# Kernel tuning notes

Hardware: AMD Instinct MI355X
Metric: run time of the kernel (lower is better)

Reference implementation:

```python
import jax, jax.numpy as jnp
import numpy as np
import math

DIM = 4096
N_HEADS = 32
N_KV_HEADS = 8
HEAD_DIM = DIM // N_HEADS  # 128
N_REP = N_HEADS // N_KV_HEADS  # 4
BATCH = 1
SEQ = 2048
ROPE_THETA = 10000.0


def setup_inputs() -> dict:
    key = jax.random.key(0)
    ks = jax.random.split(key, 6)
    x = jax.random.normal(ks[0], (BATCH, SEQ, DIM), dtype=jnp.float32)
    # torch nn.Linear weights are [out_features, in_features]
    s = 1.0 / math.sqrt(DIM)
    wq = jax.random.normal(ks[1], (N_HEADS * HEAD_DIM, DIM), dtype=jnp.float32) * s
    wk = jax.random.normal(ks[2], (N_KV_HEADS * HEAD_DIM, DIM), dtype=jnp.float32) * s
    wv = jax.random.normal(ks[3], (N_KV_HEADS * HEAD_DIM, DIM), dtype=jnp.float32) * s
    wo = jax.random.normal(ks[4], (DIM, N_HEADS * HEAD_DIM), dtype=jnp.float32) * s
    # precomputed rotary frequencies (real/imag parts of freqs_cis)
    inv_freq = 1.0 / (ROPE_THETA ** (jnp.arange(0, HEAD_DIM, 2, dtype=jnp.float32) / HEAD_DIM))
    t = jnp.arange(SEQ, dtype=jnp.float32)
    freqs = jnp.outer(t, inv_freq)  # [S, HEAD_DIM//2]
    return {"x": x, "wq": wq, "wk": wk, "wv": wv, "wo": wo,
            "freqs_cos": jnp.cos(freqs), "freqs_sin": jnp.sin(freqs)}


def _apply_rotary(t, cos, sin):
    # t: [B, S, H, HD]; cos/sin: [S, HD//2]
    B, S, H, HD = t.shape
    tr = t.reshape(B, S, H, HD // 2, 2)
    re, im = tr[..., 0], tr[..., 1]
    c = cos[None, :, None, :]
    s = sin[None, :, None, :]
    out_re = re * c - im * s
    out_im = re * s + im * c
    return jnp.stack([out_re, out_im], axis=-1).reshape(B, S, H, HD)


def reference(x, wq, wk, wv, wo, freqs_cos, freqs_sin):
    B, S, _ = x.shape
    q = jnp.einsum('bsd,od->bso', x, wq).reshape(B, S, N_HEADS, HEAD_DIM)
    k = jnp.einsum('bsd,od->bso', x, wk).reshape(B, S, N_KV_HEADS, HEAD_DIM)
    v = jnp.einsum('bsd,od->bso', x, wv).reshape(B, S, N_KV_HEADS, HEAD_DIM)
    q = _apply_rotary(q, freqs_cos, freqs_sin)
    k = _apply_rotary(k, freqs_cos, freqs_sin)
    # repeat kv heads (GQA): [B,S,Hkv,HD] -> [B,S,H,HD]
    k = jnp.repeat(k, N_REP, axis=2)
    v = jnp.repeat(v, N_REP, axis=2)
    # SDPA with causal mask
    scale = 1.0 / math.sqrt(HEAD_DIM)
    scores = jnp.einsum('bqhd,bkhd->bhqk', q, k) * scale
    causal = jnp.tril(jnp.ones((S, S), dtype=bool))
    scores = jnp.where(causal[None, None], scores, jnp.finfo(scores.dtype).min)
    attn = jax.nn.softmax(scores, axis=-1)
    y = jnp.einsum('bhqk,bkhd->bqhd', attn, v).reshape(B, S, N_HEADS * HEAD_DIM)
    return jnp.einsum('bso,do->bsd', y, wo)
```

## Files before the change

kernel.cpp:

```cpp
#include <hip/hip_runtime.h>
#include <hip/hip_bf16.h>
#include <stdint.h>

typedef unsigned short u16;
typedef __bf16 bf16_8 __attribute__((ext_vector_type(8)));
typedef float f32x4 __attribute__((ext_vector_type(4)));

#define SEQ 2048
#define DIM 4096
#define NH 32
#define NKV 8
#define HD 128
#define QSCALE_LOG2E 0.12753785222167917f

__device__ inline u16 f2bf(float f) {
    unsigned int u = __float_as_uint(f);
    unsigned int r = (u + 0x7fffu + ((u >> 16) & 1u)) >> 16;
    return (u16)r;
}

__device__ inline void async16(const void* g, void* l) {
    __builtin_amdgcn_global_load_lds(
        (const __attribute__((address_space(1))) void*)g,
        (__attribute__((address_space(3))) void*)l, 16, 0, 0);
}

__global__ __launch_bounds__(256) void cast_all(const float* __restrict__ x,
                                                const float* __restrict__ wq,
                                                const float* __restrict__ wk,
                                                const float* __restrict__ wv,
                                                const float* __restrict__ wo,
                                                u16* __restrict__ dst) {
    size_t i4 = (size_t)blockIdx.x * 256 + threadIdx.x;
    size_t e = i4 * 4;
    const float* src;
    size_t off;
    if (e < 8388608ull)       { src = x;  off = 0; }
    else if (e < 25165824ull) { src = wq; off = 8388608ull; }
    else if (e < 29360128ull) { src = wk; off = 25165824ull; }
    else if (e < 33554432ull) { src = wv; off = 29360128ull; }
    else                      { src = wo; off = 33554432ull; }
    float4 v = ((const float4*)src)[i4 - off / 4];
    ushort4 o;
    o.x = f2bf(v.x); o.y = f2bf(v.y); o.z = f2bf(v.z); o.w = f2bf(v.w);
    ((ushort4*)dst)[i4] = o;
}

template <int MODE>
__global__ __launch_bounds__(512, 2) void gemm8p(const u16* __restrict__ A,
                                                 const u16* __restrict__ B,
                                                 void* __restrict__ C0,
                                                 void* __restrict__ C1,
                                                 void* __restrict__ C2,
                                                 const float* __restrict__ fc,
                                                 const float* __restrict__ fs,
                                                 int M, int N, int K) {
    extern __shared__ u16 sm[];
    u16* As = sm;
    u16* Bs = sm + 3 * 128 * 64;

    const int tid = threadIdx.x;
    const int lane = tid & 63;
    const int wid = tid >> 6;
    const int wr = wid >> 2;
    const int wc = wid & 3;
    const int quad = lane >> 4;
    const int l16 = lane & 15;

    const int nwg = gridDim.x * gridDim.y;
    int id = blockIdx.y * gridDim.x + blockIdx.x;
    int swz = (id & 7) * (nwg >> 3) + (id >> 3);
    const int bm = (swz / gridDim.x) * 128;
    const int bn = (swz % gridDim.x) * 256;

    f32x4 acc[4][4] = {};

    auto stage = [&](int sb, int t) {
        const int k0 = t << 6;
        {
            int s0 = wc * 64 + lane;
#pragma unroll
            for (int r = 0; r < 2; ++r) {
                int S = r * 256 + s0;
                int row = S >> 3, sl = S & 7;
                int ch = sl ^ (row & 7);
                const u16* g = &A[(size_t)(bm + wr * 64 + row) * K + k0 + ch * 8];
                async16(g, (void*)&As[sb * (128 * 64) + wr * (64 * 64) + S * 8]);
            }
        }
        {
            int s0 = wr * 64 + lane;
#pragma unroll
            for (int r = 0; r < 4; ++r) {
                int S = r * 128 + s0;
                int row = S >> 3, sl = S & 7;
                int ch = sl ^ (row & 7);
                const u16* g = &B[(size_t)(bn + wc * 64 + row) * K + k0 + ch * 8];
                async16(g, (void*)&Bs[sb * (256 * 64) + wc * (64 * 64) + S * 8]);
            }
        }
    };

    const int chsw = l16 & 7;
    auto compute = [&](int p) {
        const u16* as = As + p * (128 * 64) + wr * (64 * 64);
        const u16* bs = Bs + p * (256 * 64) + wc * (64 * 64);
#pragma unroll
        for (int ks = 0; ks < 2; ++ks) {
            const int slot = ((ks * 4 + quad) ^ chsw) * 8;
            bf16_8 a[4], b[4];
#pragma unroll
            for (int i = 0; i < 4; ++i)
                a[i] = *(const bf16_8*)&as[(i * 16 + l16) * 64 + slot];
#pragma unroll
            for (int j = 0; j < 4; ++j)
                b[j] = *(const bf16_8*)&bs[(j * 16 + l16) * 64 + slot];
            __builtin_amdgcn_s_setprio(1);
#pragma unroll
            for (int i = 0; i < 4; ++i)
#pragma unroll
                for (int j = 0; j < 4; ++j)
                    acc[i][j] = __builtin_amdgcn_mfma_f32_16x16x32_bf16(a[i], b[j], acc[i][j], 0, 0, 0);
            __builtin_amdgcn_s_setprio(0);
        }
    };

    const int NT = K >> 6;
    stage(0, 0);
    stage(1, 1);

    int p = 0;
    for (int t = 0; t < NT - 2; ++t) {
        int sb = p + 2; if (sb >= 3) sb -= 3;
        stage(sb, t + 2);
        asm volatile("s_waitcnt vmcnt(12)" ::: "memory");
        __builtin_amdgcn_s_barrier();
        compute(p);
        __builtin_amdgcn_s_barrier();
        p = (p == 2) ? 0 : p + 1;
    }
    asm volatile("s_waitcnt vmcnt(6)" ::: "memory");
    __builtin_amdgcn_s_barrier();
    compute(p);
    __builtin_amdgcn_s_barrier();
    p = (p == 2) ? 0 : p + 1;
    asm volatile("s_waitcnt vmcnt(0)" ::: "memory");
    __builtin_amdgcn_s_barrier();
    compute(p);

    const int wm = wr * 64;
    const int wn = wc * 64;

    if (MODE == 0) {
        float* Cf = (float*)C0;
#pragma unroll
        for (int i = 0; i < 4; ++i)
#pragma unroll
            for (int j = 0; j < 4; ++j)
#pragma unroll
                for (int r = 0; r < 4; ++r)
                    Cf[(size_t)(bm + wm + i * 16 + quad * 4 + r) * N + (bn + wn + j * 16 + l16)] =
                        acc[i][j][r];
    } else {
        u16* Qb = (u16*)C0;
        u16* Kb = (u16*)C1;
        u16* Vt = (u16*)C2;
        if (bn < 5120) {
            const bool isQ = bn < 4096;
            const float osc = isQ ? QSCALE_LOG2E : 1.0f;
#pragma unroll
            for (int i = 0; i < 4; ++i)
#pragma unroll
                for (int j = 0; j < 4; ++j) {
                    int n = bn + wn + j * 16 + l16;
                    int pp = (n & 127) >> 1;
                    bool odd = (l16 & 1);
#pragma unroll
                    for (int r = 0; r < 4; ++r) {
                        int m = bm + wm + i * 16 + quad * 4 + r;
                        float v = acc[i][j][r];
                        float u = __shfl_xor(v, 1);
                        float c = fc[m * 64 + pp];
                        float s = fs[m * 64 + pp];
                        float o = (odd ? (u * s + v * c) : (v * c - u * s)) * osc;
                        if (isQ)
                            Qb[(size_t)m * 4096 + n] = f2bf(o);
                        else
                            Kb[(size_t)m * 1024 + (n - 4096)] = f2bf(o);
                    }
                }
        } else {
#pragma unroll
            for (int i = 0; i < 4; ++i)
#pragma unroll
                for (int j = 0; j < 4; ++j) {
                    int n = bn + wn + j * 16 + l16;
                    ushort4 o;
                    o.x = f2bf(acc[i][j][0]);
                    o.y = f2bf(acc[i][j][1]);
                    o.z = f2bf(acc[i][j][2]);
                    o.w = f2bf(acc[i][j][3]);
                    *(ushort4*)&Vt[(size_t)(n - 5120) * SEQ + (bm + wm + i * 16 + quad * 4)] = o;
                }
        }
    }
}

__global__ __launch_bounds__(256, 4) void attn_k(const u16* __restrict__ Q,
                                                 const u16* __restrict__ Kb,
                                                 const u16* __restrict__ Vt,
                                                 u16* __restrict__ Y) {
    __shared__ u16 Ks[64 * 128];
    __shared__ u16 Vs[128 * 64];
    __shared__ u16 Ps[4 * 16 * 64];
    const int tid = threadIdx.x;
    const int lane = tid & 63;
    const int w = tid >> 6;
    const int quad = lane >> 4;
    const int l16 = lane & 15;
    const int id = blockIdx.x;
    const int qt = 31 - (id >> 5);
    const int h = id & 31;
    const int kvh = h >> 2;
    const size_t qrow0 = (size_t)qt * 64;

    bf16_8 qf[4];
#pragma unroll
    for (int ks = 0; ks < 4; ++ks)
        qf[ks] = *(const bf16_8*)&Q[(qrow0 + w * 16 + l16) * DIM + h * HD + ks * 32 + quad * 8];

    f32x4 po[8] = {};
    float lsum = 0.f;

    char* psbase = (char*)Ps + w * 2048 + l16 * 128;
    const int sw = (l16 & 7) << 1;

    for (int kt = 0; kt <= qt; ++kt) {
#pragma unroll
        for (int r = 0; r < 4; ++r) {
            int S = r * 256 + tid;
            {
                int row = S >> 4, slot = S & 15;
                int chunk = slot ^ (row & 15);
                const char* g = (const char*)Kb +
                    (((size_t)kt * 64 + row) * 1024 + kvh * HD + chunk * 8) * 2;
                async16(g, (char*)Ks + S * 16);
            }
            {
                int row = S >> 3, slot = S & 7;
                int chunk = slot ^ (row & 7);
                const char* g = (const char*)Vt +
                    (((size_t)(kvh * HD + row)) * SEQ + kt * 64 + chunk * 8) * 2;
                async16(g, (char*)Vs + S * 16);
            }
        }
        __syncthreads();

        f32x4 sc[4] = {};
#pragma unroll
        for (int ks = 0; ks < 4; ++ks)
#pragma unroll
            for (int jb = 0; jb < 4; ++jb) {
                bf16_8 kb = *(const bf16_8*)&Ks[(jb * 16 + l16) * 128 + ((ks * 4 + quad) ^ l16) * 8];
                sc[jb] = __builtin_amdgcn_mfma_f32_16x16x32_bf16(kb, qf[ks], sc[jb], 0, 0, 0);
            }

        float pv[4][4];
#pragma unroll
        for (int jb = 0; jb < 4; ++jb)
#pragma unroll
            for (int r = 0; r < 4; ++r)
                pv[jb][r] = exp2f(sc[jb][r]);

        if (kt == qt) {
            int qloc = w * 16 + l16;
#pragma unroll
            for (int jb = 0; jb < 4; ++jb)
#pragma unroll
                for (int r = 0; r < 4; ++r)
                    if (jb * 16 + quad * 4 + r > qloc) pv[jb][r] = 0.f;
        }

#pragma unroll
        for (int jb = 0; jb < 4; ++jb) {
            lsum += (pv[jb][0] + pv[jb][1]) + (pv[jb][2] + pv[jb][3]);
            ushort4 pk;
            pk.x = f2bf(pv[jb][0]);
            pk.y = f2bf(pv[jb][1]);
            pk.z = f2bf(pv[jb][2]);
            pk.w = f2bf(pv[jb][3]);
            int c = jb * 4 + quad;
            *(ushort4*)(psbase + ((c ^ sw) << 3)) = pk;
        }

#pragma unroll
        for (int ks = 0; ks < 2; ++ks) {
            int c = ks * 8 + quad * 2;
            bf16_8 pf = *(const bf16_8*)(psbase + ((c ^ sw) << 3));
#pragma unroll
            for (int n = 0; n < 8; ++n) {
                bf16_8 vf = *(const bf16_8*)&Vs[(n * 16 + l16) * 64 + (((ks * 4 + quad) ^ (l16 & 7))) * 8];
                po[n] = __builtin_amdgcn_mfma_f32_16x16x32_bf16(pf, vf, po[n], 0, 0, 0);
            }
        }
        __syncthreads();
    }

    lsum += __shfl_xor(lsum, 16);
    lsum += __shfl_xor(lsum, 32);
    float inv = 1.f / lsum;
#pragma unroll
    for (int r = 0; r < 4; ++r) {
        float invr = __shfl(inv, quad * 4 + r);
        size_t row = qrow0 + w * 16 + quad * 4 + r;
#pragma unroll
        for (int n = 0; n < 8; ++n)
            Y[row * DIM + h * HD + n * 16 + l16] = f2bf(po[n][r] * invr);
    }
}

extern "C" void kernel_launch(void* const* d_in, const int* in_sizes, int n_in,
                              void* d_out, int out_size, void* d_ws, size_t ws_size,
                              hipStream_t stream) {
    const float* x  = (const float*)d_in[0];
    const float* wq = (const float*)d_in[1];
    const float* wk = (const float*)d_in[2];
    const float* wv = (const float*)d_in[3];
    const float* wo = (const float*)d_in[4];
    const float* fc = (const float*)d_in[5];
    const float* fs = (const float*)d_in[6];

    char* ws = (char*)d_ws;
    const size_t MB = 1u << 20;
    u16* xb    = (u16*)(ws);
    u16* wqkvb = (u16*)(ws + 16 * MB);
    u16* wob   = (u16*)(ws + 64 * MB);
    u16* Qb    = (u16*)(ws + 96 * MB);
    u16* Kb    = (u16*)(ws + 112 * MB);
    u16* Vtb   = (u16*)(ws + 116 * MB);
    u16* Yb    = (u16*)(ws + 120 * MB);

    const int smbytes = 3 * (128 * 64 + 256 * 64) * 2;
    static int inited = 0;
    if (!inited) {
        hipFuncSetAttribute(reinterpret_cast<const void*>(&gemm8p<1>),
                            hipFuncAttributeMaxDynamicSharedMemorySize, smbytes);
        hipFuncSetAttribute(reinterpret_cast<const void*>(&gemm8p<0>),
                            hipFuncAttributeMaxDynamicSharedMemorySize, smbytes);
        inited = 1;
    }

    cast_all<<<49152, 256, 0, stream>>>(x, wq, wk, wv, wo, (u16*)ws);

    gemm8p<1><<<dim3(24, 16), 512, smbytes, stream>>>(xb, wqkvb, Qb, Kb, Vtb, fc, fs,
                                                      2048, 6144, 4096);

    attn_k<<<dim3(1024), 256, 0, stream>>>(Qb, Kb, Vtb, Yb);

    gemm8p<0><<<dim3(16, 16), 512, smbytes, stream>>>(Yb, wob, (float*)d_out, nullptr, nullptr,
                                                      nullptr, nullptr, 2048, 4096, 4096);
}
```

Before: 506.7 us.

## Enlarge GEMM tiles to 256x256 with double-buffered four-phase interleaved staging

The bf16 GEMM block tile grows from 128x256 to 256x256, so each wave holds an 8x4 accumulator set and reuses operands more from LDS. The K loop drops from a 3-stage ring to 2 buffers, and the next tile's loads are split into four phases that alternate with MFMA work on quarter-tiles. This cuts global traffic per flop and the number of barriers per K step. In exchange the grid halves (192 and 128 blocks on a GPU with many CUs), which lowers occupancy and leaves some CUs idle, and register pressure goes up.

Result: no change. 507.0 us (+0.1%).

```diff
diff --git a/kernel.cpp b/kernel.cpp
--- a/kernel.cpp
+++ b/kernel.cpp
@@ -57,7 +57,7 @@
                                                  int M, int N, int K) {
     extern __shared__ u16 sm[];
     u16* As = sm;
-    u16* Bs = sm + 3 * 128 * 64;
+    u16* Bs = sm + 2 * 256 * 64;
 
     const int tid = threadIdx.x;
     const int lane = tid & 63;
@@ -70,91 +70,101 @@
     const int nwg = gridDim.x * gridDim.y;
     int id = blockIdx.y * gridDim.x + blockIdx.x;
     int swz = (id & 7) * (nwg >> 3) + (id >> 3);
-    const int bm = (swz / gridDim.x) * 128;
+    const int bm = (swz / gridDim.x) * 256;
     const int bn = (swz % gridDim.x) * 256;
 
-    f32x4 acc[4][4] = {};
-
-    auto stage = [&](int sb, int t) {
+    f32x4 acc[8][4] = {};
+
+    auto stageB = [&](int t, int h) {
         const int k0 = t << 6;
-        {
-            int s0 = wc * 64 + lane;
-#pragma unroll
-            for (int r = 0; r < 2; ++r) {
-                int S = r * 256 + s0;
-                int row = S >> 3, sl = S & 7;
-                int ch = sl ^ (row & 7);
-                const u16* g = &A[(size_t)(bm + wr * 64 + row) * K + k0 + ch * 8];
-                async16(g, (void*)&As[sb * (128 * 64) + wr * (64 * 64) + S * 8]);
-            }
-        }
-        {
-            int s0 = wr * 64 + lane;
-#pragma unroll
-            for (int r = 0; r < 4; ++r) {
-                int S = r * 128 + s0;
-                int row = S >> 3, sl = S & 7;
-                int ch = sl ^ (row & 7);
-                const u16* g = &B[(size_t)(bn + wc * 64 + row) * K + k0 + ch * 8];
-                async16(g, (void*)&Bs[sb * (256 * 64) + wc * (64 * 64) + S * 8]);
-            }
+        const int buf = t & 1;
+#pragma unroll
+        for (int r = 0; r < 2; ++r) {
+            int S = r * 512 + tid;
+            int row = h * 128 + (S >> 3);
+            int ch = (S & 7) ^ (row & 7);
+            const u16* g = &B[(size_t)(bn + row) * K + k0 + ch * 8];
+            async16(g, (void*)&Bs[buf * 16384 + row * 64 + (S & 7) * 8]);
         }
     };
+    auto stageA = [&](int t, int qq) {
+        const int k0 = t << 6;
+        const int buf = t & 1;
+#pragma unroll
+        for (int r = 0; r < 2; ++r) {
+            int row = r * 128 + qq * 64 + (tid >> 3);
+            int ch = (tid & 7) ^ (row & 7);
+            const u16* g = &A[(size_t)(bm + row) * K + k0 + ch * 8];
+            async16(g, (void*)&As[buf * 16384 + row * 64 + (tid & 7) * 8]);
+        }
+    };
 
     const int chsw = l16 & 7;
-    auto compute = [&](int p) {
-        const u16* as = As + p * (128 * 64) + wr * (64 * 64);
-        const u16* bs = Bs + p * (256 * 64) + wc * (64 * 64);
-#pragma unroll
-        for (int ks = 0; ks < 2; ++ks) {
-            const int slot = ((ks * 4 + quad) ^ chsw) * 8;
-            bf16_8 a[4], b[4];
-#pragma unroll
-            for (int i = 0; i < 4; ++i)
-                a[i] = *(const bf16_8*)&as[(i * 16 + l16) * 64 + slot];
-#pragma unroll
-            for (int j = 0; j < 4; ++j)
-                b[j] = *(const bf16_8*)&bs[(j * 16 + l16) * 64 + slot];
-            __builtin_amdgcn_s_setprio(1);
-#pragma unroll
-            for (int i = 0; i < 4; ++i)
-#pragma unroll
-                for (int j = 0; j < 4; ++j)
-                    acc[i][j] = __builtin_amdgcn_mfma_f32_16x16x32_bf16(a[i], b[j], acc[i][j], 0, 0, 0);
-            __builtin_amdgcn_s_setprio(0);
-        }
-    };
+    bf16_8 bfr[4][2];
+
+#define PHASE(qq, STAGE_STMT, VM_STMT)                                          \
+    {                                                                           \
+        STAGE_STMT;                                                             \
+        VM_STMT;                                                                \
+        asm volatile("s_barrier" ::: "memory");                                 \
+        if (qq == 0) {                                                          \
+            _Pragma("unroll")                                                   \
+            for (int j = 0; j < 4; ++j)                                         \
+                _Pragma("unroll")                                               \
+                for (int kk = 0; kk < 2; ++kk)                                  \
+                    bfr[j][kk] = *(const bf16_8*)&bs[(j * 16 + l16) * 64 +      \
+                                                     (((kk * 4 + quad) ^ chsw) << 3)]; \
+        }                                                                       \
+        bf16_8 afr[2][2];                                                       \
+        _Pragma("unroll")                                                       \
+        for (int i = 0; i < 2; ++i)                                             \
+            _Pragma("unroll")                                                   \
+            for (int kk = 0; kk < 2; ++kk)                                      \
+                afr[i][kk] = *(const bf16_8*)&as[((qq * 2 + i) * 16 + l16) * 64 + \
+                                                 (((kk * 4 + quad) ^ chsw) << 3)]; \
+        __builtin_amdgcn_s_setprio(1);                                          \
+        _Pragma("unroll")                                                       \
+        for (int kk = 0; kk < 2; ++kk)                                          \
+            _Pragma("unroll")                                                   \
+            for (int i = 0; i < 2; ++i)                                         \
+                _Pragma("unroll")                                               \
+                for (int j = 0; j < 4; ++j)                                     \
+                    acc[qq * 2 + i][j] = __builtin_amdgcn_mfma_f32_16x16x32_bf16( \
+                        afr[i][kk], bfr[j][kk], acc[qq * 2 + i][j], 0, 0, 0);   \
+        __builtin_amdgcn_s_setprio(0);                                          \
+    }
 
     const int NT = K >> 6;
-    stage(0, 0);
-    stage(1, 1);
-
-    int p = 0;
-    for (int t = 0; t < NT - 2; ++t) {
-        int sb = p + 2; if (sb >= 3) sb -= 3;
-        stage(sb, t + 2);
-        asm volatile("s_waitcnt vmcnt(12)" ::: "memory");
-        __builtin_amdgcn_s_barrier();
-        compute(p);
-        __builtin_amdgcn_s_barrier();
-        p = (p == 2) ? 0 : p + 1;
-    }
-    asm volatile("s_waitcnt vmcnt(6)" ::: "memory");
-    __builtin_amdgcn_s_barrier();
-    compute(p);
-    __builtin_amdgcn_s_barrier();
-    p = (p == 2) ? 0 : p + 1;
-    asm volatile("s_waitcnt vmcnt(0)" ::: "memory");
-    __builtin_amdgcn_s_barrier();
-    compute(p);
-
-    const int wm = wr * 64;
+
+    stageB(0, 0); stageB(0, 1); stageA(0, 0); stageA(0, 1);
+
+    for (int t = 0; t < NT - 1; ++t) {
+        const int buf = t & 1;
+        const u16* as = As + buf * 16384 + wr * (128 * 64);
+        const u16* bs = Bs + buf * 16384 + wc * (64 * 64);
+        PHASE(0, stageB(t + 1, 0), asm volatile("s_waitcnt vmcnt(4)" ::: "memory"))
+        PHASE(1, stageB(t + 1, 1), )
+        PHASE(2, stageA(t + 1, 0), asm volatile("s_waitcnt vmcnt(6)" ::: "memory"))
+        PHASE(3, stageA(t + 1, 1), )
+    }
+    {
+        const int buf = (NT - 1) & 1;
+        const u16* as = As + buf * 16384 + wr * (128 * 64);
+        const u16* bs = Bs + buf * 16384 + wc * (64 * 64);
+        PHASE(0, , asm volatile("s_waitcnt vmcnt(2)" ::: "memory"))
+        PHASE(1, , )
+        PHASE(2, , asm volatile("s_waitcnt vmcnt(0)" ::: "memory"))
+        PHASE(3, , )
+    }
+#undef PHASE
+
+    const int wm = wr * 128;
     const int wn = wc * 64;
 
     if (MODE == 0) {
         float* Cf = (float*)C0;
 #pragma unroll
-        for (int i = 0; i < 4; ++i)
+        for (int i = 0; i < 8; ++i)
 #pragma unroll
             for (int j = 0; j < 4; ++j)
 #pragma unroll
@@ -169,7 +179,7 @@
             const bool isQ = bn < 4096;
             const float osc = isQ ? QSCALE_LOG2E : 1.0f;
 #pragma unroll
-            for (int i = 0; i < 4; ++i)
+            for (int i = 0; i < 8; ++i)
 #pragma unroll
                 for (int j = 0; j < 4; ++j) {
                     int n = bn + wn + j * 16 + l16;
@@ -191,7 +201,7 @@
                 }
         } else {
 #pragma unroll
-            for (int i = 0; i < 4; ++i)
+            for (int i = 0; i < 8; ++i)
 #pragma unroll
                 for (int j = 0; j < 4; ++j) {
                     int n = bn + wn + j * 16 + l16;
@@ -340,7 +350,7 @@
     u16* Vtb   = (u16*)(ws + 116 * MB);
     u16* Yb    = (u16*)(ws + 120 * MB);
 
-    const int smbytes = 3 * (128 * 64 + 256 * 64) * 2;
+    const int smbytes = 4 * 256 * 64 * 2;
     static int inited = 0;
     if (!inited) {
         hipFuncSetAttribute(reinterpret_cast<const void*>(&gemm8p<1>),
@@ -352,11 +362,11 @@
 
     cast_all<<<49152, 256, 0, stream>>>(x, wq, wk, wv, wo, (u16*)ws);
 
-    gemm8p<1><<<dim3(24, 16), 512, smbytes, stream>>>(xb, wqkvb, Qb, Kb, Vtb, fc, fs,
-                                                      2048, 6144, 4096);
+    gemm8p<1><<<dim3(24, 8), 512, smbytes, stream>>>(xb, wqkvb, Qb, Kb, Vtb, fc, fs,
+                                                     2048, 6144, 4096);
 
     attn_k<<<dim3(1024), 256, 0, stream>>>(Qb, Kb, Vtb, Yb);
 
-    gemm8p<0><<<dim3(16, 16), 512, smbytes, stream>>>(Yb, wob, (float*)d_out, nullptr, nullptr,
-                                                      nullptr, nullptr, 2048, 4096, 4096);
-}
+    gemm8p<0><<<dim3(16, 8), 512, smbytes, stream>>>(Yb, wob, (float*)d_out, nullptr, nullptr,
+                                                     nullptr, nullptr, 2048, 4096, 4096);
+}
```

## Replace async-LDS triple-buffered GEMM with register-staged double-buffered 128x128 tiles

Applied to the files above, without the earlier changes.

The GEMM kernel drops direct global-to-LDS async loads with a 3-stage 128x256 tile pipeline. In its place it loads 128x128 tiles with K-step 32 into registers and writes them to padded LDS rows (stride 40) with double buffering. Blocks shrink to 256 threads with occupancy 3 and a grid twice as large, and static shared memory replaces the dynamic-size attribute setup. The aim is better occupancy and simpler bank-conflict avoidance. The cost is less reuse per tile, more barriers per K step, and register-staging overhead.

Result: slower. 1.198 ms (+136.5%).

```diff
diff --git a/kernel.cpp b/kernel.cpp
--- a/kernel.cpp
+++ b/kernel.cpp
@@ -46,24 +46,24 @@
     ((ushort4*)dst)[i4] = o;
 }
 
+#define LROW 40
 template <int MODE>
-__global__ __launch_bounds__(512, 2) void gemm8p(const u16* __restrict__ A,
-                                                 const u16* __restrict__ B,
-                                                 void* __restrict__ C0,
-                                                 void* __restrict__ C1,
-                                                 void* __restrict__ C2,
-                                                 const float* __restrict__ fc,
-                                                 const float* __restrict__ fs,
-                                                 int M, int N, int K) {
-    extern __shared__ u16 sm[];
-    u16* As = sm;
-    u16* Bs = sm + 3 * 128 * 64;
+__global__ __launch_bounds__(256, 3) void gemm_rs(const u16* __restrict__ A,
+                                                  const u16* __restrict__ B,
+                                                  void* __restrict__ C0,
+                                                  void* __restrict__ C1,
+                                                  void* __restrict__ C2,
+                                                  const float* __restrict__ fc,
+                                                  const float* __restrict__ fs,
+                                                  int M, int N, int K) {
+    __shared__ u16 As[2 * 128 * LROW];
+    __shared__ u16 Bs[2 * 128 * LROW];
 
     const int tid = threadIdx.x;
     const int lane = tid & 63;
     const int wid = tid >> 6;
-    const int wr = wid >> 2;
-    const int wc = wid & 3;
+    const int wr = wid >> 1;
+    const int wc = wid & 1;
     const int quad = lane >> 4;
     const int l16 = lane & 15;
 
@@ -71,85 +71,78 @@
     int id = blockIdx.y * gridDim.x + blockIdx.x;
     int swz = (id & 7) * (nwg >> 3) + (id >> 3);
     const int bm = (swz / gridDim.x) * 128;
-    const int bn = (swz % gridDim.x) * 256;
+    const int bn = (swz % gridDim.x) * 128;
 
     f32x4 acc[4][4] = {};
 
-    auto stage = [&](int sb, int t) {
-        const int k0 = t << 6;
-        {
-            int s0 = wc * 64 + lane;
-#pragma unroll
-            for (int r = 0; r < 2; ++r) {
-                int S = r * 256 + s0;
-                int row = S >> 3, sl = S & 7;
-                int ch = sl ^ (row & 7);
-                const u16* g = &A[(size_t)(bm + wr * 64 + row) * K + k0 + ch * 8];
-                async16(g, (void*)&As[sb * (128 * 64) + wr * (64 * 64) + S * 8]);
-            }
-        }
-        {
-            int s0 = wr * 64 + lane;
-#pragma unroll
-            for (int r = 0; r < 4; ++r) {
-                int S = r * 128 + s0;
-                int row = S >> 3, sl = S & 7;
-                int ch = sl ^ (row & 7);
-                const u16* g = &B[(size_t)(bn + wc * 64 + row) * K + k0 + ch * 8];
-                async16(g, (void*)&Bs[sb * (256 * 64) + wc * (64 * 64) + S * 8]);
-            }
-        }
+    const int srow = tid >> 1;
+    const int shalf = tid & 1;
+
+    auto gload = [&](int t, uint4* rA, uint4* rB) {
+        const int k0 = t << 5;
+        const size_t ar = (size_t)(bm + srow) * K + k0 + shalf * 16;
+        rA[0] = *(const uint4*)&A[ar];
+        rA[1] = *(const uint4*)&A[ar + 8];
+        const size_t br = (size_t)(bn + srow) * K + k0 + shalf * 16;
+        rB[0] = *(const uint4*)&B[br];
+        rB[1] = *(const uint4*)&B[br + 8];
     };
-
-    const int chsw = l16 & 7;
-    auto compute = [&](int p) {
-        const u16* as = As + p * (128 * 64) + wr * (64 * 64);
-        const u16* bs = Bs + p * (256 * 64) + wc * (64 * 64);
-#pragma unroll
-        for (int ks = 0; ks < 2; ++ks) {
-            const int slot = ((ks * 4 + quad) ^ chsw) * 8;
-            bf16_8 a[4], b[4];
-#pragma unroll
-            for (int i = 0; i < 4; ++i)
-                a[i] = *(const bf16_8*)&as[(i * 16 + l16) * 64 + slot];
-#pragma unroll
-            for (int j = 0; j < 4; ++j)
-                b[j] = *(const bf16_8*)&bs[(j * 16 + l16) * 64 + slot];
-            __builtin_amdgcn_s_setprio(1);
-#pragma unroll
-            for (int i = 0; i < 4; ++i)
-#pragma unroll
-                for (int j = 0; j < 4; ++j)
-                    acc[i][j] = __builtin_amdgcn_mfma_f32_16x16x32_bf16(a[i], b[j], acc[i][j], 0, 0, 0);
-            __builtin_amdgcn_s_setprio(0);
-        }
+    auto lwrite = [&](int buf, const uint4* rA, const uint4* rB) {
+        u16* pa = &As[buf * (128 * LROW) + srow * LROW + shalf * 16];
+        *(uint4*)&pa[0] = rA[0];
+        *(uint4*)&pa[8] = rA[1];
+        u16* pb = &Bs[buf * (128 * LROW) + srow * LROW + shalf * 16];
+        *(uint4*)&pb[0] = rB[0];
+        *(uint4*)&pb[8] = rB[1];
     };
-
-    const int NT = K >> 6;
-    stage(0, 0);
-    stage(1, 1);
-
-    int p = 0;
-    for (int t = 0; t < NT - 2; ++t) {
-        int sb = p + 2; if (sb >= 3) sb -= 3;
-        stage(sb, t + 2);
-        asm volatile("s_waitcnt vmcnt(12)" ::: "memory");
-        __builtin_amdgcn_s_barrier();
-        compute(p);
-        __builtin_amdgcn_s_barrier();
-        p = (p == 2) ? 0 : p + 1;
-    }
-    asm volatile("s_waitcnt vmcnt(6)" ::: "memory");
-    __builtin_amdgcn_s_barrier();
-    compute(p);
-    __builtin_amdgcn_s_barrier();
-    p = (p == 2) ? 0 : p + 1;
-    asm volatile("s_waitcnt vmcnt(0)" ::: "memory");
-    __builtin_amdgcn_s_barrier();
-    compute(p);
-
     const int wm = wr * 64;
     const int wn = wc * 64;
+    auto compute = [&](int buf) {
+        const u16* as = &As[buf * (128 * LROW)];
+        const u16* bs = &Bs[buf * (128 * LROW)];
+        bf16_8 a[4], b[4];
+#pragma unroll
+        for (int i = 0; i < 4; ++i)
+            a[i] = *(const bf16_8*)&as[(wm + i * 16 + l16) * LROW + quad * 8];
+#pragma unroll
+        for (int j = 0; j < 4; ++j)
+            b[j] = *(const bf16_8*)&bs[(wn + j * 16 + l16) * LROW + quad * 8];
+        __builtin_amdgcn_s_setprio(1);
+#pragma unroll
+        for (int i = 0; i < 4; ++i)
+#pragma unroll
+            for (int j = 0; j < 4; ++j)
+                acc[i][j] = __builtin_amdgcn_mfma_f32_16x16x32_bf16(a[i], b[j], acc[i][j], 0, 0, 0);
+        __builtin_amdgcn_s_setprio(0);
+    };
+
+#define LGKM_BAR()                                             \
+    asm volatile("s_waitcnt lgkmcnt(0)" ::: "memory");         \
+    __builtin_amdgcn_s_barrier()
+
+    const int NT = K >> 5;
+    uint4 ra0[2], rb0[2], ra1[2], rb1[2];
+
+    gload(0, ra0, rb0);
+    lwrite(0, ra0, rb0);
+    gload(1, ra1, rb1);
+    LGKM_BAR();
+
+    for (int t = 0; t < NT - 2; t += 2) {
+        compute(0);
+        gload(t + 2, ra0, rb0);
+        lwrite(1, ra1, rb1);
+        LGKM_BAR();
+        compute(1);
+        gload(t + 3, ra1, rb1);
+        lwrite(0, ra0, rb0);
+        LGKM_BAR();
+    }
+    compute(0);
+    lwrite(1, ra1, rb1);
+    LGKM_BAR();
+    compute(1);
+#undef LGKM_BAR
 
     if (MODE == 0) {
         float* Cf = (float*)C0;
@@ -340,23 +333,13 @@
     u16* Vtb   = (u16*)(ws + 116 * MB);
     u16* Yb    = (u16*)(ws + 120 * MB);
 
-    const int smbytes = 3 * (128 * 64 + 256 * 64) * 2;
-    static int inited = 0;
-    if (!inited) {
-        hipFuncSetAttribute(reinterpret_cast<const void*>(&gemm8p<1>),
-                            hipFuncAttributeMaxDynamicSharedMemorySize, smbytes);
-        hipFuncSetAttribute(reinterpret_cast<const void*>(&gemm8p<0>),
-                            hipFuncAttributeMaxDynamicSharedMemorySize, smbytes);
-        inited = 1;
-    }
-
     cast_all<<<49152, 256, 0, stream>>>(x, wq, wk, wv, wo, (u16*)ws);
 
-    gemm8p<1><<<dim3(24, 16), 512, smbytes, stream>>>(xb, wqkvb, Qb, Kb, Vtb, fc, fs,
-                                                      2048, 6144, 4096);
+    gemm_rs<1><<<dim3(48, 16), 256, 0, stream>>>(xb, wqkvb, Qb, Kb, Vtb, fc, fs,
+                                                 2048, 6144, 4096);
 
     attn_k<<<dim3(1024), 256, 0, stream>>>(Qb, Kb, Vtb, Yb);
 
-    gemm8p<0><<<dim3(16, 16), 512, smbytes, stream>>>(Yb, wob, (float*)d_out, nullptr, nullptr,
-                                                      nullptr, nullptr, 2048, 4096, 4096);
-}
+    gemm_rs<0><<<dim3(32, 16), 256, 0, stream>>>(Yb, wob, (float*)d_out, nullptr, nullptr,
+                                                 nullptr, nullptr, 2048, 4096, 4096);
+}
```
